# Performance work log

Hardware: AMD Instinct MI355X
Metric: run time of the kernel (lower is better)

The kernel has to match this reference:

```python
import jax, jax.numpy as jnp
import numpy as np

B, S, D = 8, 4096, 512
EPS = 1e-6


def setup_inputs() -> dict:
    key = jax.random.key(0)
    ks = jax.random.split(key, 9)
    scale = 1.0 / np.sqrt(D)
    inp = {
        "x_seq": jax.random.normal(ks[0], (B, S, D), dtype=jnp.float32),
        "Wq": jax.random.uniform(ks[1], (D, D), jnp.float32, -scale, scale),
        "bq": jax.random.uniform(ks[2], (D,), jnp.float32, -scale, scale),
        "Wk": jax.random.uniform(ks[3], (D, D), jnp.float32, -scale, scale),
        "bk": jax.random.uniform(ks[4], (D,), jnp.float32, -scale, scale),
        "Wv": jax.random.uniform(ks[5], (D, D), jnp.float32, -scale, scale),
        "bv": jax.random.uniform(ks[6], (D,), jnp.float32, -scale, scale),
        "Wa": jax.random.uniform(ks[7], (D, D), jnp.float32, -scale, scale),
        "ba": jax.random.uniform(ks[8], (D,), jnp.float32, -scale, scale),
    }
    return inp


def _forward(x_seq, Wq, bq, Wk, bk, Wv, bv, Wa, ba):
    # Precompute all projections for the whole sequence (big GEMMs).
    q = jax.nn.relu(jnp.einsum('bsd,ed->bse', x_seq, Wq) + bq)  # phi = relu
    k = jax.nn.relu(jnp.einsum('bsd,ed->bse', x_seq, Wk) + bk)
    v = jnp.einsum('bsd,ed->bse', x_seq, Wv) + bv
    a = jax.nn.sigmoid(jnp.einsum('bsd,ed->bse', x_seq, Wa) + ba)

    # time-major for scan: (S, B, D)
    qs, ks_, vs, as_ = (jnp.swapaxes(t, 0, 1) for t in (q, k, v, a))

    def step(carry, inp):
        s, z = carry                      # s: (B,D,D), z: (B,D)
        q_t, k_t, v_t, a_t = inp
        s = a_t[:, :, None] * s + k_t[:, :, None] * v_t[:, None, :]
        z = a_t * z + k_t
        num = jnp.einsum('bi,bij->bj', q_t, s)
        den = jnp.sum(q_t * z, axis=-1, keepdims=True) + EPS
        return (s, z), num / den

    s0 = jnp.zeros((x_seq.shape[0], x_seq.shape[2], x_seq.shape[2]), x_seq.dtype)
    z0 = jnp.zeros((x_seq.shape[0], x_seq.shape[2]), x_seq.dtype)
    _, ys = jax.lax.scan(step, (s0, z0), (qs, ks_, vs, as_))
    return jnp.swapaxes(ys, 0, 1)  # (B, S, D)


def reference(x_seq, Wq, bq, Wk, bk, Wv, bv, Wa, ba):
    return _forward(x_seq, Wq, bq, Wk, bk, Wv, bv, Wa, ba)
```

## Files before the change

kernel.cpp:

```cpp
#include <hip/hip_runtime.h>
#include <hip/hip_bf16.h>
#include <cstdint>
#include <cstddef>

#define D_DIM 512
#define B_DIM 8
#define S_DIM 4096
#define M_DIM (B_DIM * S_DIM)
#define CHUNK 64
#define NCHUNK (S_DIM / CHUNK)
#define NSEG 8
#define CSEG (NCHUNK / NSEG)
#define EPS_C 1e-6f

typedef __attribute__((ext_vector_type(8))) short bf16x8;
typedef __attribute__((ext_vector_type(4))) float f32x4;

__device__ __forceinline__ unsigned short f2bf(float f) {
  uint32_t u = __float_as_uint(f);
  u = (u + 0x7fffu + ((u >> 16) & 1u)) >> 16;
  return (unsigned short)u;
}
__device__ __forceinline__ float bf2f(unsigned short s) { return __uint_as_float(((uint32_t)s) << 16); }

__global__ void cvt_f32_bf16(const float* __restrict__ in, unsigned short* __restrict__ out, int n4) {
  int i = blockIdx.x * blockDim.x + threadIdx.x;
  int stride = gridDim.x * blockDim.x;
  for (; i < n4; i += stride) {
    float4 f = ((const float4*)in)[i];
    ushort4 o;
    o.x = f2bf(f.x); o.y = f2bf(f.y); o.z = f2bf(f.z); o.w = f2bf(f.w);
    ((ushort4*)out)[i] = o;
  }
}

#define TM 128
#define TN 128
#define BK 32

__global__ __launch_bounds__(256) void proj_gemm(
    const unsigned short* __restrict__ Xb,
    const unsigned short* __restrict__ Wb,
    const float* __restrict__ bq, const float* __restrict__ bk,
    const float* __restrict__ bv, const float* __restrict__ ba,
    unsigned short* __restrict__ q_ws, unsigned short* __restrict__ k_ws,
    unsigned short* __restrict__ v_ws, unsigned short* __restrict__ g_ws) {
  __shared__ unsigned short As[TM * BK];
  __shared__ unsigned short Bs[TN * BK];

  const int proj = blockIdx.z;
  const unsigned short* W = Wb + (size_t)proj * D_DIM * D_DIM;
  const int m0 = blockIdx.x * TM;
  const int n0 = blockIdx.y * TN;
  const int tid = threadIdx.x;
  const int lane = tid & 63;
  const int wave = tid >> 6;
  const int wm = (wave & 1) * 64;
  const int wn = (wave >> 1) * 64;
  const int quad = lane >> 4;
  const int l16 = lane & 15;

  f32x4 acc[4][4];
#pragma unroll
  for (int i = 0; i < 4; ++i)
#pragma unroll
    for (int j = 0; j < 4; ++j) acc[i][j] = (f32x4){0.f, 0.f, 0.f, 0.f};

  const int rw = lane >> 2;
  const int kq = (lane & 3) * 8;

  for (int kc = 0; kc < D_DIM; kc += BK) {
    __syncthreads();
    {
      const unsigned short* gA0 = &Xb[(size_t)(m0 + wave * 16 + rw) * D_DIM + kc + kq];
      const unsigned short* gA1 = &Xb[(size_t)(m0 + 64 + wave * 16 + rw) * D_DIM + kc + kq];
      const unsigned short* gB0 = &W[(size_t)(n0 + wave * 16 + rw) * D_DIM + kc + kq];
      const unsigned short* gB1 = &W[(size_t)(n0 + 64 + wave * 16 + rw) * D_DIM + kc + kq];
      __builtin_amdgcn_global_load_lds(
          (const __attribute__((address_space(1))) void*)gA0,
          (__attribute__((address_space(3))) void*)&As[(wave * 16) * BK], 16, 0, 0);
      __builtin_amdgcn_global_load_lds(
          (const __attribute__((address_space(1))) void*)gA1,
          (__attribute__((address_space(3))) void*)&As[(64 + wave * 16) * BK], 16, 0, 0);
      __builtin_amdgcn_global_load_lds(
          (const __attribute__((address_space(1))) void*)gB0,
          (__attribute__((address_space(3))) void*)&Bs[(wave * 16) * BK], 16, 0, 0);
      __builtin_amdgcn_global_load_lds(
          (const __attribute__((address_space(1))) void*)gB1,
          (__attribute__((address_space(3))) void*)&Bs[(64 + wave * 16) * BK], 16, 0, 0);
    }
    __syncthreads();

    bf16x8 afr[4], bfr[4];
#pragma unroll
    for (int im = 0; im < 4; ++im)
      afr[im] = *(const bf16x8*)&As[(wm + im * 16 + l16) * BK + quad * 8];
#pragma unroll
    for (int in = 0; in < 4; ++in)
      bfr[in] = *(const bf16x8*)&Bs[(wn + in * 16 + l16) * BK + quad * 8];
#pragma unroll
    for (int im = 0; im < 4; ++im)
#pragma unroll
      for (int in = 0; in < 4; ++in)
        acc[im][in] = __builtin_amdgcn_mfma_f32_16x16x32_bf16(afr[im], bfr[in], acc[im][in], 0, 0, 0);
  }

  const float* bias = (proj == 0) ? bq : (proj == 1) ? bk : (proj == 2) ? bv : ba;
#pragma unroll
  for (int in = 0; in < 4; ++in) {
    int nn = n0 + wn + in * 16 + l16;
    float bn = bias[nn];
#pragma unroll
    for (int im = 0; im < 4; ++im) {
      int mmb = m0 + wm + im * 16 + quad * 4;
#pragma unroll
      for (int vv = 0; vv < 4; ++vv) {
        float val = acc[im][in][vv] + bn;
        size_t idx = (size_t)(mmb + vv) * D_DIM + nn;
        if (proj == 0) {
          q_ws[idx] = f2bf(fmaxf(val, 0.f));
        } else if (proj == 1) {
          k_ws[idx] = f2bf(fmaxf(val, 0.f));
        } else if (proj == 2) {
          v_ws[idx] = f2bf(val);
        } else {
          g_ws[idx] = f2bf(val);
        }
      }
    }
  }
}

__global__ __launch_bounds__(512) void prep(
    const unsigned short* q, const unsigned short* k, const unsigned short* g,
    unsigned short* qt, unsigned short* kt, unsigned short* kh,
    float* Af, float* khs) {
  const int c = blockIdx.x, b = blockIdx.y;
  const int i = threadIdx.x;
  const size_t t0 = (size_t)b * S_DIM + (size_t)c * CHUNK;
  float cum = 1.f;
  for (int r = 0; r < CHUNK; ++r) {
    float gv = bf2f(g[(t0 + r) * D_DIM + i]);
    cum *= 1.f / (1.f + __expf(-gv));
  }
  const float cum63 = cum;
  const size_t cb = ((size_t)b * NCHUNK + c) * D_DIM;
  Af[cb + i] = cum63;
  cum = 1.f;
  float s = 0.f;
  for (int r = 0; r < CHUNK; ++r) {
    size_t idx = (t0 + r) * D_DIM + i;
    float gv = bf2f(g[idx]);
    cum *= 1.f / (1.f + __expf(-gv));
    float qv = bf2f(q[idx]);
    float kv = bf2f(k[idx]);
    qt[idx] = f2bf(qv * cum);
    float inv = 1.f / cum;
    kt[idx] = f2bf(kv * inv);
    float khf = kv * (cum63 * inv);
    kh[idx] = f2bf(khf);
    s += khf;
  }
  khs[cb + i] = s;
}

__global__ __launch_bounds__(256) void transpose_cd(
    const unsigned short* __restrict__ in, unsigned short* __restrict__ outT) {
  __shared__ unsigned short tile[CHUNK][264];
  const int c = blockIdx.x, b = blockIdx.y;
  const size_t base_in = ((size_t)b * S_DIM + (size_t)c * CHUNK) * D_DIM;
  const size_t base_out = ((size_t)b * NCHUNK + c) * (size_t)D_DIM * CHUNK;
  const int tid = threadIdx.x;
#pragma unroll
  for (int h = 0; h < 2; ++h) {
    if (h) __syncthreads();
#pragma unroll
    for (int it = 0; it < 8; ++it) {
      int flat = (it * 256 + tid) * 8;
      int row = flat >> 8;
      int col = flat & 255;
      *(uint4*)&tile[row][col] = *(const uint4*)&in[base_in + (size_t)row * D_DIM + h * 256 + col];
    }
    __syncthreads();
#pragma unroll
    for (int it = 0; it < 8; ++it) {
      int wq = it * 256 + tid;
      int i_loc = wq >> 3;
      int r0 = (wq & 7) * 8;
      ushort4 v0, v1;
      v0.x = tile[r0 + 0][i_loc]; v0.y = tile[r0 + 1][i_loc];
      v0.z = tile[r0 + 2][i_loc]; v0.w = tile[r0 + 3][i_loc];
      v1.x = tile[r0 + 4][i_loc]; v1.y = tile[r0 + 5][i_loc];
      v1.z = tile[r0 + 6][i_loc]; v1.w = tile[r0 + 7][i_loc];
      size_t o = base_out + (size_t)(h * 256 + i_loc) * CHUNK + r0;
      *(ushort4*)&outT[o] = v0;
      *(ushort4*)&outT[o + 4] = v1;
    }
  }
}

__global__ __launch_bounds__(256) void intra(
    const unsigned short* __restrict__ qt, const unsigned short* kt,
    const unsigned short* __restrict__ VT,
    unsigned short* numI, float* __restrict__ rs) {
  __shared__ unsigned short P_lds[CHUNK][CHUNK + 8];
  const int c = blockIdx.x, b = blockIdx.y;
  const size_t t0 = (size_t)b * S_DIM + (size_t)c * CHUNK;
  const int lane = threadIdx.x & 63, w = threadIdx.x >> 6;
  const int l16 = lane & 15, q4 = lane >> 4;

  f32x4 accP[4];
#pragma unroll
  for (int n = 0; n < 4; ++n) accP[n] = (f32x4){0.f, 0.f, 0.f, 0.f};
#pragma unroll
  for (int ks = 0; ks < 16; ++ks) {
    bf16x8 afr = *(const bf16x8*)&qt[(t0 + 16 * w + l16) * D_DIM + 32 * ks + 8 * q4];
#pragma unroll
    for (int n = 0; n < 4; ++n) {
      bf16x8 bfr = *(const bf16x8*)&kt[(t0 + 16 * n + l16) * D_DIM + 32 * ks + 8 * q4];
      accP[n] = __builtin_amdgcn_mfma_f32_16x16x32_bf16(afr, bfr, accP[n], 0, 0, 0);
    }
  }
  float rsum[4] = {0.f, 0.f, 0.f, 0.f};
#pragma unroll
  for (int n = 0; n < 4; ++n) {
    int m = 16 * n + l16;
#pragma unroll
    for (int vv = 0; vv < 4; ++vv) {
      int r = 16 * w + 4 * q4 + vv;
      float pv = (m <= r) ? accP[n][vv] : 0.f;
      rsum[vv] += pv;
      P_lds[r][m] = f2bf(pv);
    }
  }
#pragma unroll
  for (int msk = 1; msk < 16; msk <<= 1) {
#pragma unroll
    for (int vv = 0; vv < 4; ++vv) rsum[vv] += __shfl_xor(rsum[vv], msk, 64);
  }
  if (l16 == 0) {
#pragma unroll
    for (int vv = 0; vv < 4; ++vv) rs[t0 + 16 * w + 4 * q4 + vv] = rsum[vv];
  }
  __syncthreads();
  bf16x8 pa0 = *(const bf16x8*)&P_lds[16 * w + l16][8 * q4];
  bf16x8 pa1 = *(const bf16x8*)&P_lds[16 * w + l16][32 + 8 * q4];
  const size_t vtb = ((size_t)b * NCHUNK + c) * (size_t)D_DIM * CHUNK;
#pragma unroll 4
  for (int nt = 0; nt < 32; ++nt) {
    bf16x8 b0 = *(const bf16x8*)&VT[vtb + (size_t)(nt * 16 + l16) * CHUNK + 8 * q4];
    bf16x8 b1 = *(const bf16x8*)&VT[vtb + (size_t)(nt * 16 + l16) * CHUNK + 32 + 8 * q4];
    f32x4 acc = (f32x4){0.f, 0.f, 0.f, 0.f};
    acc = __builtin_amdgcn_mfma_f32_16x16x32_bf16(pa0, b0, acc, 0, 0, 0);
    acc = __builtin_amdgcn_mfma_f32_16x16x32_bf16(pa1, b1, acc, 0, 0, 0);
#pragma unroll
    for (int vv = 0; vv < 4; ++vv)
      numI[(t0 + 16 * w + 4 * q4 + vv) * D_DIM + nt * 16 + l16] = f2bf(acc[vv]);
  }
}

__global__ __launch_bounds__(512) void zscan(
    const float* __restrict__ Af, const float* __restrict__ khs,
    float* __restrict__ zall, float* __restrict__ Pseg) {
  const int b = blockIdx.x;
  const int i = threadIdx.x;
  float z = 0.f, rp = 1.f;
  for (int c = 0; c < NCHUNK; ++c) {
    const size_t cb = ((size_t)b * NCHUNK + c) * D_DIM;
    zall[cb + i] = z;
    float af = Af[cb + i];
    z = fmaf(af, z, khs[cb + i]);
    rp *= af;
    if ((c & (CSEG - 1)) == CSEG - 1) {
      Pseg[((size_t)b * NSEG + (c / CSEG)) * D_DIM + i] = rp;
      rp = 1.f;
    }
  }
}

__global__ __launch_bounds__(512) void denk(
    const unsigned short* __restrict__ qt, const float* __restrict__ zall,
    float* rs_invden) {
  const int c = blockIdx.x, b = blockIdx.y;
  const int lane = threadIdx.x & 63, w = threadIdx.x >> 6;
  const size_t t0 = (size_t)b * S_DIM + (size_t)c * CHUNK;
  const size_t zb = ((size_t)b * NCHUNK + c) * D_DIM;
  float4 z0 = *(const float4*)&zall[zb + lane * 8];
  float4 z1 = *(const float4*)&zall[zb + lane * 8 + 4];
#pragma unroll
  for (int rr = 0; rr < 8; ++rr) {
    int r = 8 * w + rr;
    bf16x8 qv = *(const bf16x8*)&qt[(t0 + r) * D_DIM + lane * 8];
    float p = 0.f;
    p = fmaf(bf2f((unsigned short)qv[0]), z0.x, p);
    p = fmaf(bf2f((unsigned short)qv[1]), z0.y, p);
    p = fmaf(bf2f((unsigned short)qv[2]), z0.z, p);
    p = fmaf(bf2f((unsigned short)qv[3]), z0.w, p);
    p = fmaf(bf2f((unsigned short)qv[4]), z1.x, p);
    p = fmaf(bf2f((unsigned short)qv[5]), z1.y, p);
    p = fmaf(bf2f((unsigned short)qv[6]), z1.z, p);
    p = fmaf(bf2f((unsigned short)qv[7]), z1.w, p);
#pragma unroll
    for (int msk = 1; msk < 64; msk <<= 1) p += __shfl_xor(p, msk, 64);
    if (lane == 0) {
      float* iv = &rs_invden[t0 + r];
      *iv = 1.f / (p + *iv + EPS_C);
    }
  }
}

__global__ __launch_bounds__(512, 2) void useg_k(
    const unsigned short* __restrict__ khT, const unsigned short* __restrict__ VT,
    const float* __restrict__ Af, unsigned short* __restrict__ U) {
  const int s = blockIdx.x, jt = blockIdx.y, b = blockIdx.z;
  const int lane = threadIdx.x & 63, w = threadIdx.x >> 6;
  const int l16 = lane & 15, q4 = lane >> 4;
  const int j0 = jt * 128;
  const int iw = 128 * (w & 3);
  const int jw = 64 * (w >> 2);

  f32x4 acc[8][4];
#pragma unroll
  for (int T = 0; T < 8; ++T)
#pragma unroll
    for (int h = 0; h < 4; ++h) acc[T][h] = (f32x4){0.f, 0.f, 0.f, 0.f};

  for (int cc = 0; cc < CSEG; ++cc) {
    const int c = s * CSEG + cc;
    const size_t cb = ((size_t)b * NCHUNK + c) * D_DIM;
    const size_t ob = cb * CHUNK;
#pragma unroll
    for (int T = 0; T < 8; ++T) {
      float4 af = *(const float4*)&Af[cb + iw + 16 * T + 4 * q4];
#pragma unroll
      for (int h = 0; h < 4; ++h) {
        acc[T][h][0] *= af.x; acc[T][h][1] *= af.y; acc[T][h][2] *= af.z; acc[T][h][3] *= af.w;
      }
    }
    bf16x8 bv0[4], bv1[4];
#pragma unroll
    for (int h = 0; h < 4; ++h) {
      bv0[h] = *(const bf16x8*)&VT[ob + (size_t)(j0 + jw + 16 * h + l16) * CHUNK + 8 * q4];
      bv1[h] = *(const bf16x8*)&VT[ob + (size_t)(j0 + jw + 16 * h + l16) * CHUNK + 32 + 8 * q4];
    }
#pragma unroll
    for (int T = 0; T < 8; ++T) {
      bf16x8 a0 = *(const bf16x8*)&khT[ob + (size_t)(iw + 16 * T + l16) * CHUNK + 8 * q4];
      bf16x8 a1 = *(const bf16x8*)&khT[ob + (size_t)(iw + 16 * T + l16) * CHUNK + 32 + 8 * q4];
#pragma unroll
      for (int h = 0; h < 4; ++h) {
        acc[T][h] = __builtin_amdgcn_mfma_f32_16x16x32_bf16(a0, bv0[h], acc[T][h], 0, 0, 0);
        acc[T][h] = __builtin_amdgcn_mfma_f32_16x16x32_bf16(a1, bv1[h], acc[T][h], 0, 0, 0);
      }
    }
  }
  const size_t ub = ((size_t)b * NSEG + s) * D_DIM;
#pragma unroll
  for (int T = 0; T < 8; ++T)
#pragma unroll
    for (int h = 0; h < 4; ++h) {
      uint2 pk;
      pk.x = (uint32_t)f2bf(acc[T][h][0]) | ((uint32_t)f2bf(acc[T][h][1]) << 16);
      pk.y = (uint32_t)f2bf(acc[T][h][2]) | ((uint32_t)f2bf(acc[T][h][3]) << 16);
      *(uint2*)&U[(ub + j0 + jw + 16 * h + l16) * (size_t)D_DIM + iw + 16 * T + 4 * q4] = pk;
    }
}

__global__ __launch_bounds__(256) void sscan(
    const float* __restrict__ Pseg, unsigned short* __restrict__ U) {
  const int b = blockIdx.y;
  const int flat = blockIdx.x * 256 + threadIdx.x;
  const int j = flat >> 6;
  const int i0 = (flat & 63) * 8;
  float acc[8];
#pragma unroll
  for (int t = 0; t < 8; ++t) acc[t] = 0.f;
  for (int s = 0; s < NSEG; ++s) {
    const size_t pb = ((size_t)b * NSEG + s) * D_DIM;
    unsigned short* up = &U[(pb + j) * (size_t)D_DIM + i0];
    uint4 u = *(const uint4*)up;
    float4 p0 = *(const float4*)&Pseg[pb + i0];
    float4 p1 = *(const float4*)&Pseg[pb + i0 + 4];
    float uv[8];
    uv[0] = bf2f((unsigned short)(u.x & 0xffff)); uv[1] = bf2f((unsigned short)(u.x >> 16));
    uv[2] = bf2f((unsigned short)(u.y & 0xffff)); uv[3] = bf2f((unsigned short)(u.y >> 16));
    uv[4] = bf2f((unsigned short)(u.z & 0xffff)); uv[5] = bf2f((unsigned short)(u.z >> 16));
    uv[6] = bf2f((unsigned short)(u.w & 0xffff)); uv[7] = bf2f((unsigned short)(u.w >> 16));
    uint4 o;
    o.x = (uint32_t)f2bf(acc[0]) | ((uint32_t)f2bf(acc[1]) << 16);
    o.y = (uint32_t)f2bf(acc[2]) | ((uint32_t)f2bf(acc[3]) << 16);
    o.z = (uint32_t)f2bf(acc[4]) | ((uint32_t)f2bf(acc[5]) << 16);
    o.w = (uint32_t)f2bf(acc[6]) | ((uint32_t)f2bf(acc[7]) << 16);
    *(uint4*)up = o;
    acc[0] = fmaf(p0.x, acc[0], uv[0]);
    acc[1] = fmaf(p0.y, acc[1], uv[1]);
    acc[2] = fmaf(p0.z, acc[2], uv[2]);
    acc[3] = fmaf(p0.w, acc[3], uv[3]);
    acc[4] = fmaf(p1.x, acc[4], uv[4]);
    acc[5] = fmaf(p1.y, acc[5], uv[5]);
    acc[6] = fmaf(p1.z, acc[6], uv[6]);
    acc[7] = fmaf(p1.w, acc[7], uv[7]);
  }
}

__global__ __launch_bounds__(512, 2) void scan2(
    const unsigned short* __restrict__ qt, const unsigned short* __restrict__ khT,
    const unsigned short* __restrict__ VT, const float* __restrict__ Af,
    const unsigned short* __restrict__ Sin,
    const unsigned short* __restrict__ numI, const float* __restrict__ invden,
    float* __restrict__ out) {
  __shared__ unsigned short STj[128][520];
  const int s = blockIdx.x, jt = blockIdx.y, b = blockIdx.z;
  const int lane = threadIdx.x & 63, w = threadIdx.x >> 6;
  const int l16 = lane & 15, q4 = lane >> 4;
  const int j0 = jt * 128;
  const int iw = 128 * (w & 3);
  const int jw = 64 * (w >> 2);
  const int rw = 16 * (w & 3);
  const int jo = 64 * (w >> 2);

  f32x4 acc[8][4];

  {
    const size_t pb = ((size_t)b * NSEG + s) * D_DIM;
#pragma unroll
    for (int T = 0; T < 8; ++T)
#pragma unroll
      for (int h = 0; h < 4; ++h) {
        uint2 uu = *(const uint2*)&Sin[(pb + j0 + jw + 16 * h + l16) * (size_t)D_DIM + iw + 16 * T + 4 * q4];
        acc[T][h][0] = bf2f((unsigned short)(uu.x & 0xffff));
        acc[T][h][1] = bf2f((unsigned short)(uu.x >> 16));
        acc[T][h][2] = bf2f((unsigned short)(uu.y & 0xffff));
        acc[T][h][3] = bf2f((unsigned short)(uu.y >> 16));
      }
  }

  for (int cc = 0; cc < CSEG; ++cc) {
    const int c = s * CSEG + cc;
    const size_t cb = ((size_t)b * NCHUNK + c) * D_DIM;
    const size_t t0 = (size_t)b * S_DIM + (size_t)c * CHUNK;
    const size_t ob = cb * CHUNK;

#pragma unroll
    for (int T = 0; T < 8; ++T)
#pragma unroll
      for (int h = 0; h < 4; ++h) {
        uint2 pk;
        pk.x = (uint32_t)f2bf(acc[T][h][0]) | ((uint32_t)f2bf(acc[T][h][1]) << 16);
        pk.y = (uint32_t)f2bf(acc[T][h][2]) | ((uint32_t)f2bf(acc[T][h][3]) << 16);
        *(uint2*)&STj[jw + 16 * h + l16][iw + 16 * T + 4 * q4] = pk;
      }
    __syncthreads();

    {
      f32x4 accO[4];
#pragma unroll
      for (int h = 0; h < 4; ++h) accO[h] = (f32x4){0.f, 0.f, 0.f, 0.f};
#pragma unroll
      for (int ks = 0; ks < 16; ++ks) {
        bf16x8 afr = *(const bf16x8*)&qt[(t0 + rw + l16) * D_DIM + 32 * ks + 8 * q4];
#pragma unroll
        for (int h = 0; h < 4; ++h) {
          bf16x8 bfr = *(const bf16x8*)&STj[jo + 16 * h + l16][32 * ks + 8 * q4];
          accO[h] = __builtin_amdgcn_mfma_f32_16x16x32_bf16(afr, bfr, accO[h], 0, 0, 0);
        }
      }
#pragma unroll
      for (int h = 0; h < 4; ++h)
#pragma unroll
        for (int vv = 0; vv < 4; ++vv) {
          size_t t = t0 + rw + 4 * q4 + vv;
          int j = j0 + jo + 16 * h + l16;
          float idv = invden[t];
          float nI = bf2f(numI[t * D_DIM + j]);
          out[t * D_DIM + j] = (accO[h][vv] + nI) * idv;
        }
    }

    if (cc != CSEG - 1) {
#pragma unroll
      for (int T = 0; T < 8; ++T) {
        float4 af = *(const float4*)&Af[cb + iw + 16 * T + 4 * q4];
#pragma unroll
        for (int h = 0; h < 4; ++h) {
          acc[T][h][0] *= af.x; acc[T][h][1] *= af.y; acc[T][h][2] *= af.z; acc[T][h][3] *= af.w;
        }
      }
      bf16x8 bv0[4], bv1[4];
#pragma unroll
      for (int h = 0; h < 4; ++h) {
        bv0[h] = *(const bf16x8*)&VT[ob + (size_t)(j0 + jw + 16 * h + l16) * CHUNK + 8 * q4];
        bv1[h] = *(const bf16x8*)&VT[ob + (size_t)(j0 + jw + 16 * h + l16) * CHUNK + 32 + 8 * q4];
      }
#pragma unroll
      for (int T = 0; T < 8; ++T) {
        bf16x8 a0 = *(const bf16x8*)&khT[ob + (size_t)(iw + 16 * T + l16) * CHUNK + 8 * q4];
        bf16x8 a1 = *(const bf16x8*)&khT[ob + (size_t)(iw + 16 * T + l16) * CHUNK + 32 + 8 * q4];
#pragma unroll
        for (int h = 0; h < 4; ++h) {
          acc[T][h] = __builtin_amdgcn_mfma_f32_16x16x32_bf16(a0, bv0[h], acc[T][h], 0, 0, 0);
          acc[T][h] = __builtin_amdgcn_mfma_f32_16x16x32_bf16(a1, bv1[h], acc[T][h], 0, 0, 0);
        }
      }
    }
    __syncthreads();
  }
}

extern "C" void kernel_launch(void* const* d_in, const int* in_sizes, int n_in,
                              void* d_out, int out_size, void* d_ws, size_t ws_size,
                              hipStream_t stream) {
  const float* x  = (const float*)d_in[0];
  const float* Wq = (const float*)d_in[1];
  const float* bq = (const float*)d_in[2];
  const float* Wk = (const float*)d_in[3];
  const float* bk = (const float*)d_in[4];
  const float* Wv = (const float*)d_in[5];
  const float* bv = (const float*)d_in[6];
  const float* Wa = (const float*)d_in[7];
  const float* ba = (const float*)d_in[8];
  float* out = (float*)d_out;

  const size_t MD2 = (size_t)M_DIM * D_DIM * 2;
  uint8_t* w = (uint8_t*)d_ws;
  unsigned short* xb   = (unsigned short*)w; w += MD2;
  unsigned short* wb   = (unsigned short*)w; w += (size_t)4 * D_DIM * D_DIM * 2;
  unsigned short* q_ws = (unsigned short*)w; w += MD2;
  unsigned short* k_ws = (unsigned short*)w; w += MD2;
  unsigned short* v_ws = (unsigned short*)w; w += MD2;
  unsigned short* g_ws = (unsigned short*)w; w += MD2;
  float* Af     = (float*)w; w += (size_t)B_DIM * NCHUNK * D_DIM * 4;
  float* khs    = (float*)w; w += (size_t)B_DIM * NCHUNK * D_DIM * 4;
  float* invden = (float*)w; w += (size_t)M_DIM * 4;

  unsigned short* qt   = xb;
  unsigned short* kt   = q_ws;
  unsigned short* kh   = k_ws;
  unsigned short* VT   = g_ws;
  unsigned short* khT  = v_ws;
  unsigned short* numI = q_ws;
  unsigned short* U    = k_ws;
  float* zall = (float*)wb;
  float* Pseg = (float*)((uint8_t*)wb + (1 << 20));

  cvt_f32_bf16<<<1024, 256, 0, stream>>>(x, xb, M_DIM * D_DIM / 4);
  cvt_f32_bf16<<<128, 256, 0, stream>>>(Wq, wb + 0 * D_DIM * D_DIM, D_DIM * D_DIM / 4);
  cvt_f32_bf16<<<128, 256, 0, stream>>>(Wk, wb + 1 * D_DIM * D_DIM, D_DIM * D_DIM / 4);
  cvt_f32_bf16<<<128, 256, 0, stream>>>(Wv, wb + 2 * D_DIM * D_DIM, D_DIM * D_DIM / 4);
  cvt_f32_bf16<<<128, 256, 0, stream>>>(Wa, wb + 3 * D_DIM * D_DIM, D_DIM * D_DIM / 4);

  proj_gemm<<<dim3(M_DIM / TM, D_DIM / TN, 4), 256, 0, stream>>>(
      xb, wb, bq, bk, bv, ba, q_ws, k_ws, v_ws, g_ws);

  prep<<<dim3(NCHUNK, B_DIM), 512, 0, stream>>>(q_ws, k_ws, g_ws, qt, kt, kh, Af, khs);
  transpose_cd<<<dim3(NCHUNK, B_DIM), 256, 0, stream>>>(v_ws, VT);
  transpose_cd<<<dim3(NCHUNK, B_DIM), 256, 0, stream>>>(kh, khT);
  zscan<<<B_DIM, 512, 0, stream>>>(Af, khs, zall, Pseg);
  intra<<<dim3(NCHUNK, B_DIM), 256, 0, stream>>>(qt, kt, VT, numI, invden);
  denk<<<dim3(NCHUNK, B_DIM), 512, 0, stream>>>(qt, zall, invden);
  useg_k<<<dim3(NSEG, 4, B_DIM), 512, 0, stream>>>(khT, VT, Af, U);
  sscan<<<dim3(128, B_DIM), 256, 0, stream>>>(Pseg, U);
  scan2<<<dim3(NSEG, 4, B_DIM), 512, 0, stream>>>(qt, khT, VT, Af, U, numI, invden, out);
}
```

Measured before the change: 568.7 us.

## Stage GEMM epilogue through LDS and parallelize prep over time segments

Result: faster. 530.7 us (-6.7%).

```diff
diff --git a/kernel.cpp b/kernel.cpp
--- a/kernel.cpp
+++ b/kernel.cpp
@@ -45,8 +45,9 @@
     const float* __restrict__ bv, const float* __restrict__ ba,
     unsigned short* __restrict__ q_ws, unsigned short* __restrict__ k_ws,
     unsigned short* __restrict__ v_ws, unsigned short* __restrict__ g_ws) {
-  __shared__ unsigned short As[TM * BK];
-  __shared__ unsigned short Bs[TN * BK];
+  __shared__ unsigned short SB[TM * BK + TN * BK];
+  unsigned short* As = SB;
+  unsigned short* Bs = SB + TM * BK;
 
   const int proj = blockIdx.z;
   const unsigned short* W = Wb + (size_t)proj * D_DIM * D_DIM;
@@ -105,63 +106,134 @@
         acc[im][in] = __builtin_amdgcn_mfma_f32_16x16x32_bf16(afr[im], bfr[in], acc[im][in], 0, 0, 0);
   }
 
+  __syncthreads();
+
   const float* bias = (proj == 0) ? bq : (proj == 1) ? bk : (proj == 2) ? bv : ba;
-#pragma unroll
-  for (int in = 0; in < 4; ++in) {
-    int nn = n0 + wn + in * 16 + l16;
-    float bn = bias[nn];
-#pragma unroll
-    for (int im = 0; im < 4; ++im) {
-      int mmb = m0 + wm + im * 16 + quad * 4;
-#pragma unroll
-      for (int vv = 0; vv < 4; ++vv) {
-        float val = acc[im][in][vv] + bn;
-        size_t idx = (size_t)(mmb + vv) * D_DIM + nn;
-        if (proj == 0) {
-          q_ws[idx] = f2bf(fmaxf(val, 0.f));
-        } else if (proj == 1) {
-          k_ws[idx] = f2bf(fmaxf(val, 0.f));
-        } else if (proj == 2) {
-          v_ws[idx] = f2bf(val);
-        } else {
-          g_ws[idx] = f2bf(val);
+  unsigned short* outp = (proj == 0) ? q_ws : (proj == 1) ? k_ws : (proj == 2) ? v_ws : g_ws;
+  const bool do_relu = (proj <= 1);
+  unsigned short* EP = &SB[wave * 64 * 32];
+
+#pragma unroll
+  for (int p = 0; p < 2; ++p) {
+#pragma unroll
+    for (int half = 0; half < 2; ++half) {
+      const int in = 2 * p + half;
+      const int nn = n0 + wn + in * 16 + l16;
+      const float bn = bias[nn];
+#pragma unroll
+      for (int im = 0; im < 4; ++im) {
+#pragma unroll
+        for (int vv = 0; vv < 4; ++vv) {
+          float val = acc[im][in][vv] + bn;
+          if (do_relu) val = fmaxf(val, 0.f);
+          EP[(im * 16 + quad * 4 + vv) * 32 + half * 16 + l16] = f2bf(val);
         }
       }
     }
+#pragma unroll
+    for (int it = 0; it < 4; ++it) {
+      const int row = it * 16 + (lane >> 2);
+      const int ccol = (lane & 3) * 8;
+      bf16x8 vdat = *(const bf16x8*)&EP[row * 32 + ccol];
+      size_t gidx = (size_t)(m0 + wm + row) * D_DIM + (size_t)(n0 + wn + p * 32 + ccol);
+      *(bf16x8*)&outp[gidx] = vdat;
+    }
   }
 }
 
 __global__ __launch_bounds__(512) void prep(
-    const unsigned short* q, const unsigned short* k, const unsigned short* g,
-    unsigned short* qt, unsigned short* kt, unsigned short* kh,
-    float* Af, float* khs) {
+    const unsigned short* __restrict__ q, const unsigned short* __restrict__ k,
+    const unsigned short* __restrict__ g,
+    unsigned short* __restrict__ qt, unsigned short* __restrict__ kt,
+    unsigned short* __restrict__ kh,
+    float* __restrict__ Af, float* __restrict__ khs) {
+  __shared__ float segp[8][512];
   const int c = blockIdx.x, b = blockIdx.y;
-  const int i = threadIdx.x;
+  const int seg = threadIdx.x >> 6;
+  const int t = threadIdx.x & 63;
+  const int i0 = t * 8;
+  const int r0 = seg * 8;
   const size_t t0 = (size_t)b * S_DIM + (size_t)c * CHUNK;
-  float cum = 1.f;
-  for (int r = 0; r < CHUNK; ++r) {
-    float gv = bf2f(g[(t0 + r) * D_DIM + i]);
-    cum *= 1.f / (1.f + __expf(-gv));
-  }
-  const float cum63 = cum;
   const size_t cb = ((size_t)b * NCHUNK + c) * D_DIM;
-  Af[cb + i] = cum63;
-  cum = 1.f;
-  float s = 0.f;
-  for (int r = 0; r < CHUNK; ++r) {
-    size_t idx = (t0 + r) * D_DIM + i;
-    float gv = bf2f(g[idx]);
-    cum *= 1.f / (1.f + __expf(-gv));
-    float qv = bf2f(q[idx]);
-    float kv = bf2f(k[idx]);
-    qt[idx] = f2bf(qv * cum);
-    float inv = 1.f / cum;
-    kt[idx] = f2bf(kv * inv);
-    float khf = kv * (cum63 * inv);
-    kh[idx] = f2bf(khf);
-    s += khf;
-  }
-  khs[cb + i] = s;
+
+  float sp[8];
+#pragma unroll
+  for (int j = 0; j < 8; ++j) sp[j] = 1.f;
+  for (int r = 0; r < 8; ++r) {
+    bf16x8 gv = *(const bf16x8*)&g[(t0 + r0 + r) * D_DIM + i0];
+#pragma unroll
+    for (int j = 0; j < 8; ++j)
+      sp[j] *= 1.f / (1.f + __expf(-bf2f((unsigned short)gv[j])));
+  }
+  *(float4*)&segp[seg][i0] = *(float4*)&sp[0];
+  *(float4*)&segp[seg][i0 + 4] = *(float4*)&sp[4];
+  __syncthreads();
+
+  float pre[8], tot[8];
+#pragma unroll
+  for (int j = 0; j < 8; ++j) { pre[j] = 1.f; tot[j] = 1.f; }
+  for (int s2 = 0; s2 < 8; ++s2) {
+    float4 v0 = *(const float4*)&segp[s2][i0];
+    float4 v1 = *(const float4*)&segp[s2][i0 + 4];
+    float v[8] = {v0.x, v0.y, v0.z, v0.w, v1.x, v1.y, v1.z, v1.w};
+#pragma unroll
+    for (int j = 0; j < 8; ++j) {
+      tot[j] *= v[j];
+      if (s2 < seg) pre[j] *= v[j];
+    }
+  }
+  if (seg == 0) {
+    float4 a0 = {tot[0], tot[1], tot[2], tot[3]};
+    float4 a1 = {tot[4], tot[5], tot[6], tot[7]};
+    *(float4*)&Af[cb + i0] = a0;
+    *(float4*)&Af[cb + i0 + 4] = a1;
+  }
+
+  float cum[8], ssum[8];
+#pragma unroll
+  for (int j = 0; j < 8; ++j) { cum[j] = pre[j]; ssum[j] = 0.f; }
+  for (int r = 0; r < 8; ++r) {
+    size_t idx = (t0 + r0 + r) * D_DIM + i0;
+    bf16x8 gv = *(const bf16x8*)&g[idx];
+    bf16x8 qv8 = *(const bf16x8*)&q[idx];
+    bf16x8 kv8 = *(const bf16x8*)&k[idx];
+    bf16x8 oq, ok, okh;
+#pragma unroll
+    for (int j = 0; j < 8; ++j) {
+      cum[j] *= 1.f / (1.f + __expf(-bf2f((unsigned short)gv[j])));
+      float qv = bf2f((unsigned short)qv8[j]);
+      float kv = bf2f((unsigned short)kv8[j]);
+      oq[j] = (short)f2bf(qv * cum[j]);
+      float inv = 1.f / cum[j];
+      ok[j] = (short)f2bf(kv * inv);
+      float khf = kv * (tot[j] * inv);
+      okh[j] = (short)f2bf(khf);
+      ssum[j] += khf;
+    }
+    *(bf16x8*)&qt[idx] = oq;
+    *(bf16x8*)&kt[idx] = ok;
+    *(bf16x8*)&kh[idx] = okh;
+  }
+
+  __syncthreads();
+  *(float4*)&segp[seg][i0] = *(float4*)&ssum[0];
+  *(float4*)&segp[seg][i0 + 4] = *(float4*)&ssum[4];
+  __syncthreads();
+  if (seg == 0) {
+    float s[8];
+#pragma unroll
+    for (int j = 0; j < 8; ++j) s[j] = 0.f;
+    for (int s2 = 0; s2 < 8; ++s2) {
+      float4 v0 = *(const float4*)&segp[s2][i0];
+      float4 v1 = *(const float4*)&segp[s2][i0 + 4];
+      s[0] += v0.x; s[1] += v0.y; s[2] += v0.z; s[3] += v0.w;
+      s[4] += v1.x; s[5] += v1.y; s[6] += v1.z; s[7] += v1.w;
+    }
+    float4 a0 = {s[0], s[1], s[2], s[3]};
+    float4 a1 = {s[4], s[5], s[6], s[7]};
+    *(float4*)&khs[cb + i0] = a0;
+    *(float4*)&khs[cb + i0 + 4] = a1;
+  }
 }
 
 __global__ __launch_bounds__(256) void transpose_cd(
```
